# Optimization experiments

Measured on AMD Instinct MI355X. Metric: run time of the kernel, lower is better.

## Reference

```python
import jax, jax.numpy as jnp
import numpy as np

B, N, M, C, H, W = 8, 16, 4, 2, 256, 256
GAMMA = 0.5   # gamma0
BETA = 1.0    # beta
EPS = 1e-8


def setup_inputs() -> dict:
    key = jax.random.key(0)
    k1, k2, k3, k4 = jax.random.split(key, 4)
    gt_arr = jax.random.randint(k1, (B, M, H, W), 0, C)
    sample_arr = jax.random.uniform(k2, (B, N, C, H, W), dtype=jnp.float32)
    prob = jax.random.uniform(k3, (B, N), dtype=jnp.float32)
    prob_gt = jax.random.uniform(k4, (B, M), dtype=jnp.float32)
    prob_gt = prob_gt / prob_gt.sum(-1, keepdims=True)  # gt mixture weights sum to 1
    sample_shape = jnp.array([4, 4], dtype=jnp.int64 if jax.config.read('jax_enable_x64') else jnp.int32)  # (K,S); unused since G0=1
    return {"gt_arr": gt_arr, "sample_arr": sample_arr, "prob": prob,
            "prob_gt": prob_gt, "sample_shape": sample_shape}


def _cost_iou(sample, gt_oh):
    # sample: (B,N,C,HW), gt_oh: (B,M,C,HW) -> cost (B,N,M)
    inter = jnp.einsum('bnch,bmch->bnmc', sample, gt_oh)
    union = sample.sum(-1)[:, :, None, :] + gt_oh.sum(-1)[:, None, :, :] - inter
    # drop background channel 0, mean over remaining channels
    return 1.0 - ((inter + 1.0) / (union + 1.0))[..., 1:].mean(-1)


def _coupling(cost, prob_gt):
    # Greedy sequential OT coupling (gamma != 1 branch), vectorized per gt column
    # via water-filling over cost-sorted samples; sequential over gt columns.
    Bn, Nn, Mn = cost.shape
    mass = 1.0 / Mn

    def per_batch(cb):  # cb: (N,M)
        order_gt = jnp.argsort(cb.min(axis=0))  # gts by their min cost

        def step(carry, i):
            rowsums, P = carry
            col = cb[:, i]                      # (N,)
            ordj = jnp.argsort(col)             # samples by cost for this gt
            caps = GAMMA - rowsums[ordj]        # remaining capacity, >= 0
            excl = jnp.cumsum(caps) - caps      # exclusive prefix of capacities
            a_sorted = jnp.clip(mass - excl, 0.0, caps)
            assign = jnp.zeros((Nn,), cb.dtype).at[ordj].set(a_sorted)
            P = P.at[:, i].set(assign)
            return (rowsums + assign, P), None

        init = (jnp.zeros((Nn,), cb.dtype), jnp.zeros((Nn, Mn), cb.dtype))
        (_, P), _ = jax.lax.scan(step, init, order_gt)
        return P

    P = jax.vmap(per_batch)(cost)
    return P * (prob_gt * Mn)[:, None, :]


def _forward(gt_arr, sample_arr, prob, prob_gt):
    Bn, Nn, Cn, Hn, Wn = sample_arr.shape
    Mn = gt_arr.shape[1]
    sample = sample_arr.reshape(Bn, Nn, Cn, Hn * Wn)
    gt_oh = jnp.transpose(
        jax.nn.one_hot(gt_arr.reshape(Bn, Mn, Hn * Wn), Cn, dtype=sample.dtype),
        (0, 1, 3, 2))                            # (B,M,C,HW)
    cost = _cost_iou(sample, gt_oh)              # (B,N,M)
    P = jax.lax.stop_gradient(_coupling(jax.lax.stop_gradient(cost), prob_gt))
    seg_loss = (P * cost).sum((1, 2)).mean()
    # KL: F.kl_div(log(prob+eps), target_prob) with 'mean' reduction (xlogy at 0)
    target = P.sum(-1)                           # (B,N)
    logp = jnp.log(prob + EPS)
    safe_t = jnp.where(target > 0, target, 1.0)
    kl = jnp.where(target > 0, target * (jnp.log(safe_t) - logp), 0.0).mean()
    loss = seg_loss + BETA * kl
    return loss, seg_loss, kl


def reference(gt_arr, sample_arr, prob, prob_gt, sample_shape):
    return _forward(gt_arr, sample_arr, prob, prob_gt)
```

## Files before the change

kernel.cpp:

```cpp
#include <hip/hip_runtime.h>
#include <math.h>

static constexpr int Bn = 8;
static constexpr int Nn = 16;
static constexpr int Mn = 4;
static constexpr int Cn = 2;
static constexpr int HWn = 256 * 256;
static constexpr int Sn = 16;
static constexpr int SEGLEN = HWn / Sn;
#define GAMMA_F 0.5f
#define MASS_F 0.25f
#define EPS_F 1e-8f


__global__ __launch_bounds__(256) void inter_kernel(
    const float* __restrict__ sample, const int* __restrict__ gt,
    float* __restrict__ inter_part, float* __restrict__ ssum_part,
    float* __restrict__ gsum_part) {
  int blk = blockIdx.x;
  int b = blk & 7;
  int r = blk >> 3;
  int s = r & 15;
  int n = r >> 4;

  const float* sp = sample + ((((size_t)b * Nn + n) * Cn + 1) * HWn) + (size_t)s * SEGLEN;
  const int* gtb = gt + (size_t)b * Mn * HWn + (size_t)s * SEGLEN;

  float ss = 0.f, im0 = 0.f, im1 = 0.f, im2 = 0.f, im3 = 0.f;
  unsigned int c0 = 0, c1 = 0, c2 = 0, c3 = 0;

#pragma unroll
  for (int q = 0; q < 4; ++q) {
    int i = q * 256 + threadIdx.x;
    float4 x = reinterpret_cast<const float4*>(sp)[i];
    int4 g0 = reinterpret_cast<const int4*>(gtb + 0 * HWn)[i];
    int4 g1 = reinterpret_cast<const int4*>(gtb + 1 * HWn)[i];
    int4 g2 = reinterpret_cast<const int4*>(gtb + 2 * HWn)[i];
    int4 g3 = reinterpret_cast<const int4*>(gtb + 3 * HWn)[i];
    float xs[4] = {x.x, x.y, x.z, x.w};
    int m0[4] = {g0.x, g0.y, g0.z, g0.w};
    int m1[4] = {g1.x, g1.y, g1.z, g1.w};
    int m2[4] = {g2.x, g2.y, g2.z, g2.w};
    int m3[4] = {g3.x, g3.y, g3.z, g3.w};
#pragma unroll
    for (int e = 0; e < 4; ++e) {
      float v = xs[e];
      ss += v;
      bool b0 = (m0[e] == 1), b1 = (m1[e] == 1), b2 = (m2[e] == 1), b3 = (m3[e] == 1);
      im0 += b0 ? v : 0.0f;
      im1 += b1 ? v : 0.0f;
      im2 += b2 ? v : 0.0f;
      im3 += b3 ? v : 0.0f;
      c0 += b0; c1 += b1; c2 += b2; c3 += b3;
    }
  }

#pragma unroll
  for (int off = 32; off > 0; off >>= 1) {
    ss  += __shfl_down(ss, off);
    im0 += __shfl_down(im0, off);
    im1 += __shfl_down(im1, off);
    im2 += __shfl_down(im2, off);
    im3 += __shfl_down(im3, off);
    c0  += __shfl_down(c0, off);
    c1  += __shfl_down(c1, off);
    c2  += __shfl_down(c2, off);
    c3  += __shfl_down(c3, off);
  }

  __shared__ float sred[4][5];
  __shared__ unsigned int scnt[4][4];
  int lane = threadIdx.x & 63;
  int wv = threadIdx.x >> 6;
  if (lane == 0) {
    sred[wv][0] = ss; sred[wv][1] = im0; sred[wv][2] = im1;
    sred[wv][3] = im2; sred[wv][4] = im3;
    scnt[wv][0] = c0; scnt[wv][1] = c1; scnt[wv][2] = c2; scnt[wv][3] = c3;
  }
  __syncthreads();
  if (threadIdx.x == 0) {
    float t[5] = {0, 0, 0, 0, 0};
    for (int w = 0; w < 4; ++w)
      for (int v = 0; v < 5; ++v) t[v] += sred[w][v];
    int bn = b * Nn + n;
    ssum_part[(size_t)bn * Sn + s] = t[0];
    float* ip = inter_part + ((size_t)bn * Sn + s) * Mn;
    ip[0] = t[1]; ip[1] = t[2]; ip[2] = t[3]; ip[3] = t[4];
    if (n == 0) {
      unsigned int cc[4] = {0, 0, 0, 0};
      for (int w = 0; w < 4; ++w)
        for (int m = 0; m < 4; ++m) cc[m] += scnt[w][m];
      float* gp = gsum_part + ((size_t)b * Sn + s) * Mn;
      gp[0] = (float)cc[0]; gp[1] = (float)cc[1];
      gp[2] = (float)cc[2]; gp[3] = (float)cc[3];
    }
  }
}

__global__ __launch_bounds__(256) void finish_kernel(
    const float* __restrict__ inter_part, const float* __restrict__ ssum_part,
    const float* __restrict__ gsum_part,
    const float* __restrict__ prob, const float* __restrict__ prob_gt,
    float* __restrict__ out) {
  __shared__ __align__(16) float s_im[Bn * Nn * Mn];
  __shared__ float s_ssum[Bn * Nn];
  __shared__ __align__(16) float s_gsum[Bn * Mn];
  __shared__ float s_cost[Bn * Nn * Mn];
  __shared__ float s_red[8];
  int tid = threadIdx.x;

  if (tid < Bn * Nn) {
    const float4* ip = reinterpret_cast<const float4*>(&inter_part[(size_t)tid * Sn * Mn]);
    float4 a4 = ip[0];
#pragma unroll
    for (int j = 1; j < 16; ++j) {
      float4 t = ip[j];
      a4.x += t.x; a4.y += t.y; a4.z += t.z; a4.w += t.w;
    }
    *reinterpret_cast<float4*>(&s_im[tid * Mn]) = a4;
    const float4* sp4 = reinterpret_cast<const float4*>(&ssum_part[(size_t)tid * Sn]);
    float4 s4 = sp4[0];
#pragma unroll
    for (int j = 1; j < 4; ++j) {
      float4 t = sp4[j];
      s4.x += t.x; s4.y += t.y; s4.z += t.z; s4.w += t.w;
    }
    s_ssum[tid] = (s4.x + s4.y) + (s4.z + s4.w);
  } else if (tid < 128 + Bn) {
    int b = tid - 128;
    const float4* gp = reinterpret_cast<const float4*>(&gsum_part[(size_t)b * Sn * Mn]);
    float4 a4 = gp[0];
#pragma unroll
    for (int j = 1; j < 16; ++j) {
      float4 t = gp[j];
      a4.x += t.x; a4.y += t.y; a4.z += t.z; a4.w += t.w;
    }
    *reinterpret_cast<float4*>(&s_gsum[b * Mn]) = a4;
  }
  __syncthreads();

  for (int idx = tid; idx < Bn * Nn * Mn; idx += 256) {
    int m = idx & 3;
    int bn = idx >> 2;
    int b = bn >> 4;
    float inter = s_im[idx];
    float uni = s_ssum[bn] + s_gsum[(b << 2) + m] - inter;
    s_cost[idx] = 1.0f - (inter + 1.0f) / (uni + 1.0f);
  }
  __syncthreads();

  float seg_part = 0.f, kl_part = 0.f;
  if (tid < Bn * Nn) {
    int b = tid >> 4;
    int n = tid & 15;
    int base = (tid & 63) & ~15;

    float4 cv = *reinterpret_cast<const float4*>(&s_cost[tid * Mn]);
    float cc0 = cv.x, cc1 = cv.y, cc2 = cv.z, cc3 = cv.w;
    float pg0 = prob_gt[b * Mn + 0], pg1 = prob_gt[b * Mn + 1];
    float pg2 = prob_gt[b * Mn + 2], pg3 = prob_gt[b * Mn + 3];

    float m0 = cc0, m1 = cc1, m2 = cc2, m3 = cc3;
#pragma unroll
    for (int off = 1; off < 16; off <<= 1) {
      m0 = fminf(m0, __shfl_xor(m0, off));
      m1 = fminf(m1, __shfl_xor(m1, off));
      m2 = fminf(m2, __shfl_xor(m2, off));
      m3 = fminf(m3, __shfl_xor(m3, off));
    }
    int r0 = (m1 < m0) + (m2 < m0) + (m3 < m0);
    int r1 = (m0 <= m1) + (m2 < m1) + (m3 < m1);
    int r2 = (m0 <= m2) + (m1 <= m2) + (m3 < m2);
    int r3 = (m0 <= m3) + (m1 <= m3) + (m2 <= m3);

    float rowsum = 0.f;
    float target = 0.f;
#pragma unroll
    for (int k = 0; k < Mn; ++k) {
      int i = (r0 == k) ? 0 : (r1 == k) ? 1 : (r2 == k) ? 2 : 3;
      float v = (i == 0) ? cc0 : (i == 1) ? cc1 : (i == 2) ? cc2 : cc3;
      float pg = (i == 0) ? pg0 : (i == 1) ? pg1 : (i == 2) ? pg2 : pg3;
      float cap = GAMMA_F - rowsum;
      float excl = 0.f;
#pragma unroll 4
      for (int j = 0; j < Nn; ++j) {
        float vj = __shfl(v, base + j);
        float capj = __shfl(cap, base + j);
        bool pred = (vj < v) || (vj == v && j < n);
        excl += pred ? capj : 0.f;
      }
      float a = fminf(fmaxf(MASS_F - excl, 0.f), cap);
      rowsum += a;
      float p = a * pg * (float)Mn;
      seg_part += p * v;
      target += p;
    }
    kl_part = (target > 0.f)
                  ? target * (logf(target) - logf(prob[tid] + EPS_F))
                  : 0.f;
  }

#pragma unroll
  for (int off = 32; off > 0; off >>= 1) {
    seg_part += __shfl_down(seg_part, off);
    kl_part += __shfl_down(kl_part, off);
  }
  int lane = tid & 63, wv = tid >> 6;
  if (lane == 0) { s_red[wv * 2] = seg_part; s_red[wv * 2 + 1] = kl_part; }
  __syncthreads();
  if (tid == 0) {
    float seg = 0.f, kl = 0.f;
    for (int w = 0; w < 4; ++w) { seg += s_red[w * 2]; kl += s_red[w * 2 + 1]; }
    seg /= (float)Bn;
    kl /= (float)(Bn * Nn);
    out[0] = seg + 1.0f * kl;
    out[1] = seg;
    out[2] = kl;
  }
}

extern "C" void kernel_launch(void* const* d_in, const int* in_sizes, int n_in,
                              void* d_out, int out_size, void* d_ws, size_t ws_size,
                              hipStream_t stream) {
  const int* gt = (const int*)d_in[0];
  const float* sample = (const float*)d_in[1];
  const float* prob = (const float*)d_in[2];
  const float* prob_gt = (const float*)d_in[3];
  float* out = (float*)d_out;

  char* ws = (char*)d_ws;
  float* inter_part = (float*)(ws + 0);
  float* ssum_part = (float*)(ws + 32768);
  float* gsum_part = (float*)(ws + 40960);

  inter_kernel<<<Bn * Nn * Sn, 256, 0, stream>>>(sample, gt, inter_part, ssum_part, gsum_part);
  finish_kernel<<<1, 256, 0, stream>>>(inter_part, ssum_part, gsum_part, prob, prob_gt, out);
}
```

Baseline: 22.24 us.

## Fuse finish into reduction kernel via last-block atomic counter; halve segments

```diff
diff --git a/kernel.cpp b/kernel.cpp
--- a/kernel.cpp
+++ b/kernel.cpp
@@ -6,22 +6,30 @@
 static constexpr int Mn = 4;
 static constexpr int Cn = 2;
 static constexpr int HWn = 256 * 256;
-static constexpr int Sn = 16;
+static constexpr int Sn = 8;
 static constexpr int SEGLEN = HWn / Sn;
+static constexpr int GRID = Bn * Nn * Sn;
 #define GAMMA_F 0.5f
 #define MASS_F 0.25f
 #define EPS_F 1e-8f
 
 
-__global__ __launch_bounds__(256) void inter_kernel(
+__device__ __forceinline__ float agent_load(const float* p) {
+  return __hip_atomic_load(p, __ATOMIC_RELAXED, __HIP_MEMORY_SCOPE_AGENT);
+}
+
+__global__ __launch_bounds__(256) void fused_kernel(
     const float* __restrict__ sample, const int* __restrict__ gt,
+    const float* __restrict__ prob, const float* __restrict__ prob_gt,
+    unsigned int* __restrict__ counter,
     float* __restrict__ inter_part, float* __restrict__ ssum_part,
-    float* __restrict__ gsum_part) {
+    float* __restrict__ gsum_part, float* __restrict__ out) {
   int blk = blockIdx.x;
-  int b = blk & 7;
-  int r = blk >> 3;
-  int s = r & 15;
-  int n = r >> 4;
+  int s = blk & (Sn - 1);
+  int bn = blk >> 3;
+  int n = bn & 15;
+  int b = bn >> 4;
+  int tid = threadIdx.x;
 
   const float* sp = sample + ((((size_t)b * Nn + n) * Cn + 1) * HWn) + (size_t)s * SEGLEN;
   const int* gtb = gt + (size_t)b * Mn * HWn + (size_t)s * SEGLEN;
@@ -30,8 +38,8 @@
   unsigned int c0 = 0, c1 = 0, c2 = 0, c3 = 0;
 
 #pragma unroll
-  for (int q = 0; q < 4; ++q) {
-    int i = q * 256 + threadIdx.x;
+  for (int q = 0; q < 8; ++q) {
+    int i = q * 256 + tid;
     float4 x = reinterpret_cast<const float4*>(sp)[i];
     int4 g0 = reinterpret_cast<const int4*>(gtb + 0 * HWn)[i];
     int4 g1 = reinterpret_cast<const int4*>(gtb + 1 * HWn)[i];
@@ -70,19 +78,19 @@
 
   __shared__ float sred[4][5];
   __shared__ unsigned int scnt[4][4];
-  int lane = threadIdx.x & 63;
-  int wv = threadIdx.x >> 6;
+  __shared__ unsigned int s_last;
+  int lane = tid & 63;
+  int wv = tid >> 6;
   if (lane == 0) {
     sred[wv][0] = ss; sred[wv][1] = im0; sred[wv][2] = im1;
     sred[wv][3] = im2; sred[wv][4] = im3;
     scnt[wv][0] = c0; scnt[wv][1] = c1; scnt[wv][2] = c2; scnt[wv][3] = c3;
   }
   __syncthreads();
-  if (threadIdx.x == 0) {
+  if (tid == 0) {
     float t[5] = {0, 0, 0, 0, 0};
     for (int w = 0; w < 4; ++w)
       for (int v = 0; v < 5; ++v) t[v] += sred[w][v];
-    int bn = b * Nn + n;
     ssum_part[(size_t)bn * Sn + s] = t[0];
     float* ip = inter_part + ((size_t)bn * Sn + s) * Mn;
     ip[0] = t[1]; ip[1] = t[2]; ip[2] = t[3]; ip[3] = t[4];
@@ -94,71 +102,66 @@
       gp[0] = (float)cc[0]; gp[1] = (float)cc[1];
       gp[2] = (float)cc[2]; gp[3] = (float)cc[3];
     }
-  }
-}
-
-__global__ __launch_bounds__(256) void finish_kernel(
-    const float* __restrict__ inter_part, const float* __restrict__ ssum_part,
-    const float* __restrict__ gsum_part,
-    const float* __restrict__ prob, const float* __restrict__ prob_gt,
-    float* __restrict__ out) {
+    __threadfence();
+    unsigned int old = atomicAdd(counter, 1u);
+    s_last = (old == (unsigned int)(GRID - 1)) ? 1u : 0u;
+  }
+  __syncthreads();
+  if (s_last == 0u) return;
+
+  __threadfence();
   __shared__ __align__(16) float s_im[Bn * Nn * Mn];
   __shared__ float s_ssum[Bn * Nn];
-  __shared__ __align__(16) float s_gsum[Bn * Mn];
+  __shared__ float s_gsum[Bn * Mn];
   __shared__ float s_cost[Bn * Nn * Mn];
   __shared__ float s_red[8];
-  int tid = threadIdx.x;
 
   if (tid < Bn * Nn) {
-    const float4* ip = reinterpret_cast<const float4*>(&inter_part[(size_t)tid * Sn * Mn]);
-    float4 a4 = ip[0];
-#pragma unroll
-    for (int j = 1; j < 16; ++j) {
-      float4 t = ip[j];
-      a4.x += t.x; a4.y += t.y; a4.z += t.z; a4.w += t.w;
-    }
-    *reinterpret_cast<float4*>(&s_im[tid * Mn]) = a4;
-    const float4* sp4 = reinterpret_cast<const float4*>(&ssum_part[(size_t)tid * Sn]);
-    float4 s4 = sp4[0];
-#pragma unroll
-    for (int j = 1; j < 4; ++j) {
-      float4 t = sp4[j];
-      s4.x += t.x; s4.y += t.y; s4.z += t.z; s4.w += t.w;
-    }
-    s_ssum[tid] = (s4.x + s4.y) + (s4.z + s4.w);
-  } else if (tid < 128 + Bn) {
-    int b = tid - 128;
-    const float4* gp = reinterpret_cast<const float4*>(&gsum_part[(size_t)b * Sn * Mn]);
-    float4 a4 = gp[0];
-#pragma unroll
-    for (int j = 1; j < 16; ++j) {
-      float4 t = gp[j];
-      a4.x += t.x; a4.y += t.y; a4.z += t.z; a4.w += t.w;
-    }
-    *reinterpret_cast<float4*>(&s_gsum[b * Mn]) = a4;
+    float a0 = 0.f, a1 = 0.f, a2 = 0.f, a3 = 0.f, sv = 0.f;
+    const float* ip = inter_part + (size_t)tid * Sn * Mn;
+    const float* sp2 = ssum_part + (size_t)tid * Sn;
+#pragma unroll
+    for (int j = 0; j < Sn; ++j) {
+      a0 += agent_load(ip + j * 4 + 0);
+      a1 += agent_load(ip + j * 4 + 1);
+      a2 += agent_load(ip + j * 4 + 2);
+      a3 += agent_load(ip + j * 4 + 3);
+      sv += agent_load(sp2 + j);
+    }
+    s_im[tid * Mn + 0] = a0; s_im[tid * Mn + 1] = a1;
+    s_im[tid * Mn + 2] = a2; s_im[tid * Mn + 3] = a3;
+    s_ssum[tid] = sv;
+  } else if (tid < 128 + Bn * Mn) {
+    int idx = tid - 128;
+    int bb = idx >> 2, m = idx & 3;
+    float g = 0.f;
+    const float* gp = gsum_part + (size_t)bb * Sn * Mn + m;
+#pragma unroll
+    for (int j = 0; j < Sn; ++j) g += agent_load(gp + j * 4);
+    s_gsum[idx] = g;
   }
   __syncthreads();
 
   for (int idx = tid; idx < Bn * Nn * Mn; idx += 256) {
     int m = idx & 3;
-    int bn = idx >> 2;
-    int b = bn >> 4;
+    int bnn = idx >> 2;
+    int bb = bnn >> 4;
     float inter = s_im[idx];
-    float uni = s_ssum[bn] + s_gsum[(b << 2) + m] - inter;
+    float uni = s_ssum[bnn] + s_gsum[(bb << 2) + m] - inter;
     s_cost[idx] = 1.0f - (inter + 1.0f) / (uni + 1.0f);
   }
   __syncthreads();
 
   float seg_part = 0.f, kl_part = 0.f;
   if (tid < Bn * Nn) {
-    int b = tid >> 4;
-    int n = tid & 15;
+    int bb = tid >> 4;
+    int nn = tid & 15;
     int base = (tid & 63) & ~15;
 
     float4 cv = *reinterpret_cast<const float4*>(&s_cost[tid * Mn]);
     float cc0 = cv.x, cc1 = cv.y, cc2 = cv.z, cc3 = cv.w;
-    float pg0 = prob_gt[b * Mn + 0], pg1 = prob_gt[b * Mn + 1];
-    float pg2 = prob_gt[b * Mn + 2], pg3 = prob_gt[b * Mn + 3];
+    float pg0 = prob_gt[bb * Mn + 0], pg1 = prob_gt[bb * Mn + 1];
+    float pg2 = prob_gt[bb * Mn + 2], pg3 = prob_gt[bb * Mn + 3];
 
     float m0 = cc0, m1 = cc1, m2 = cc2, m3 = cc3;
 #pragma unroll
@@ -186,7 +189,7 @@
       for (int j = 0; j < Nn; ++j) {
         float vj = __shfl(v, base + j);
         float capj = __shfl(cap, base + j);
-        bool pred = (vj < v) || (vj == v && j < n);
+        bool pred = (vj < v) || (vj == v && j < nn);
         excl += pred ? capj : 0.f;
       }
       float a = fminf(fmaxf(MASS_F - excl, 0.f), cap);
@@ -205,7 +208,6 @@
     seg_part += __shfl_down(seg_part, off);
     kl_part += __shfl_down(kl_part, off);
   }
-  int lane = tid & 63, wv = tid >> 6;
   if (lane == 0) { s_red[wv * 2] = seg_part; s_red[wv * 2 + 1] = kl_part; }
   __syncthreads();
   if (tid == 0) {
@@ -229,10 +231,12 @@
   float* out = (float*)d_out;
 
   char* ws = (char*)d_ws;
-  float* inter_part = (float*)(ws + 0);
-  float* ssum_part = (float*)(ws + 32768);
-  float* gsum_part = (float*)(ws + 40960);
-
-  inter_kernel<<<Bn * Nn * Sn, 256, 0, stream>>>(sample, gt, inter_part, ssum_part, gsum_part);
-  finish_kernel<<<1, 256, 0, stream>>>(inter_part, ssum_part, gsum_part, prob, prob_gt, out);
+  unsigned int* counter = (unsigned int*)(ws + 0);
+  float* inter_part = (float*)(ws + 256);
+  float* ssum_part = (float*)(ws + 16640);
+  float* gsum_part = (float*)(ws + 20736);
+
+  hipMemsetAsync(counter, 0, sizeof(unsigned int), stream);
+  fused_kernel<<<GRID, 256, 0, stream>>>(sample, gt, prob, prob_gt, counter,
+                                         inter_part, ssum_part, gsum_part, out);
 }
```

Result: slower. 53.85 us (+142.1%).
